# Optimization experiments

Measured on AMD Instinct MI355X. Metric: run time of the kernel, lower is better.

The kernel has to match this reference:

```python
import jax, jax.numpy as jnp
import numpy as np

N_HEADS = 16
EMBED = 1024
T = 2048        # given tokens
CACHE_NUM = 1024  # prepended cache tokens (x[0,-1] in the original)


def setup_inputs() -> dict:
    key = jax.random.key(0)
    k1, k2 = jax.random.split(key)
    qkv = jax.random.normal(k1, (T, 3 * EMBED), dtype=jnp.float32)
    # In the original these cache rows are torch.randn generated inside forward;
    # we lift them into a deterministic explicit input with identical semantics.
    cache = jax.random.normal(k2, (CACHE_NUM, 3 * EMBED), dtype=jnp.float32)
    return {"qkv": qkv, "cache": cache}


def reference(qkv, cache):
    C = EMBED
    H = N_HEADS
    D = C // H  # head_dim = 64
    t = qkv.shape[0]
    tc = cache.shape[0]
    t_full = t + tc  # T_ in the original

    gq, gk, gv = jnp.split(qkv, 3, axis=1)      # each [T, C]
    cq, ck, cv = jnp.split(cache, 3, axis=1)    # each [cache_num, C]

    q = jnp.concatenate([cq, gq], axis=0)  # [T_, C]
    k = jnp.concatenate([ck, gk], axis=0)
    v = jnp.concatenate([cv, gv], axis=0)

    # [T_, C] -> [H, T_, D]
    q = q.reshape(t_full, H, D).transpose(1, 0, 2)
    k = k.reshape(t_full, H, D).transpose(1, 0, 2)
    v = v.reshape(t_full, H, D).transpose(1, 0, 2)

    scale = 1.0 / np.sqrt(D).astype(np.float32)
    att = jnp.einsum('htd,hsd->hts', q, k) * scale  # [H, T_, T_]

    causal = jnp.tril(jnp.ones((t_full, t_full), dtype=bool))
    att = jnp.where(causal[None, :, :], att, jnp.float32(-jnp.inf))
    att = jax.nn.softmax(att, axis=-1)
    # attn_dropout is identity in eval / p=0

    y = jnp.einsum('hts,hsd->htd', att, v)          # [H, T_, D]
    y = y.transpose(1, 0, 2).reshape(t_full, C)     # [T_, C]
    return y[tc:, :]                                # drop cache rows -> [T, C]
```

## Files before the change

### kernel.cpp

```cpp
#include <hip/hip_runtime.h>
#include <cmath>


typedef _Float16 f16;
typedef __attribute__((ext_vector_type(8))) _Float16 f16x8;
typedef __attribute__((ext_vector_type(4))) _Float16 f16x4;
typedef __attribute__((ext_vector_type(2))) _Float16 f16x2;
typedef __attribute__((ext_vector_type(4))) float    f32x4;

constexpr int TC  = 1024;
constexpr int C3  = 3072;
constexpr int CE  = 1024;
constexpr int NH  = 16;
constexpr int TQ  = 2048;
constexpr int NKT = 48;

constexpr size_t KV_ELEMS = (size_t)NH * NKT * 4096;

constexpr int SPLITS[16] = {2,2,3,3,3,3,4,4,4,4,5,5,5,5,6,6};
constexpr int PRE[16]    = {0,2,4,7,10,13,16,20,24,28,32,37,42,47,52,58};
constexpr int NSLOT      = 64;

constexpr size_t OPART_E = (size_t)NSLOT * NH * 128 * 64;
constexpr size_t LPART_F = (size_t)NSLOT * NH * 128;

__device__ __forceinline__ void dma16(const void* g, void* l) {
    __builtin_amdgcn_global_load_lds(
        (const __attribute__((address_space(1))) void*)g,
        (__attribute__((address_space(3))) void*)l, 16, 0, 0);
}

__device__ __forceinline__ f16x2 pkrtz(float a, float b) {
    return __builtin_bit_cast(f16x2, __builtin_amdgcn_cvt_pkrtz(a, b));
}

__global__ __launch_bounds__(256)
void prepass_f16(const float* __restrict__ qkv, const float* __restrict__ cache,
                 f16* __restrict__ Kt, f16* __restrict__ Vt)
{
    const int b   = blockIdx.x;
    const int h   = b & 15;
    const int kt  = b >> 4;
    const int tid = threadIdx.x;
    const int bt  = kt * 64;
    const float* src = (bt < TC) ? (cache + (size_t)bt * C3)
                                 : (qkv + (size_t)(bt - TC) * C3);
    f16* ktile = Kt + (size_t)(h * NKT + kt) * 4096;
    f16* vtile = Vt + (size_t)(h * NKT + kt) * 4096;

    __shared__ f16 vtmp[64 * 66];

    {
        const int tok = tid >> 2;
        const int c4  = tid & 3;
        const float* p = src + (size_t)tok * C3 + h * 64 + CE + c4 * 16;
        f32x4 x0 = ((const f32x4*)p)[0], x1 = ((const f32x4*)p)[1];
        f32x4 x2 = ((const f32x4*)p)[2], x3 = ((const f32x4*)p)[3];
        const int ch0 = (2 * c4)     ^ (tok & 7);
        const int ch1 = (2 * c4 + 1) ^ (tok & 7);
        *(f16x8*)&ktile[tok * 64 + ch0 * 8] =
            (f16x8){(f16)x0.x,(f16)x0.y,(f16)x0.z,(f16)x0.w,
                    (f16)x1.x,(f16)x1.y,(f16)x1.z,(f16)x1.w};
        *(f16x8*)&ktile[tok * 64 + ch1 * 8] =
            (f16x8){(f16)x2.x,(f16)x2.y,(f16)x2.z,(f16)x2.w,
                    (f16)x3.x,(f16)x3.y,(f16)x3.z,(f16)x3.w};
    }
    {
        const int tok  = tid >> 2;
        const int dblk = (tid & 3) * 16;
        const float* p = src + (size_t)tok * C3 + h * 64 + 2 * CE + dblk;
        f32x4 x0 = ((const f32x4*)p)[0], x1 = ((const f32x4*)p)[1];
        f32x4 x2 = ((const f32x4*)p)[2], x3 = ((const f32x4*)p)[3];
        float v[16] = {x0.x,x0.y,x0.z,x0.w, x1.x,x1.y,x1.z,x1.w,
                       x2.x,x2.y,x2.z,x2.w, x3.x,x3.y,x3.z,x3.w};
        f16* dst = &vtmp[tok * 66 + dblk];
        #pragma unroll
        for (int i = 0; i < 8; ++i)
            *(f16x2*)&dst[2 * i] = (f16x2){(f16)v[2 * i], (f16)v[2 * i + 1]};
    }
    __syncthreads();
    {
        const int d  = tid >> 2;
        const int tb = (tid & 3) * 16;
        f16 col[16];
        #pragma unroll
        for (int i = 0; i < 16; ++i) col[i] = vtmp[(tb + i) * 66 + d];
        const int c0 = tb >> 3;
        *(f16x8*)&vtile[d * 64 + ((c0 ^ (d & 7)) * 8)] =
            (f16x8){col[0],col[1],col[2],col[3],col[4],col[5],col[6],col[7]};
        *(f16x8*)&vtile[d * 64 + (((c0 + 1) ^ (d & 7)) * 8)] =
            (f16x8){col[8],col[9],col[10],col[11],col[12],col[13],col[14],col[15]};
    }
}

__device__ __forceinline__ void tile_loop(
    const char* kg, const char* vg, int t0, int t1, int qbase_w,
    int l15, int quad, int ksw, int soff,
    const f16x8 (&qfrag)[2][2], f16 (&sKV)[2][8192],
    f32x4 (&o_accT)[2][4], float (&l_i)[2])
{
    {
        char* kl = (char*)&sKV[0][0]    + soff;
        char* vl = (char*)&sKV[0][4096] + soff;
        dma16(kg, kl);           dma16(kg + 1024, kl + 1024);
        dma16(vg, vl);           dma16(vg + 1024, vl + 1024);
    }
    int cur = 0;

    for (int kt = t0; kt < t1; ++kt) {
        asm volatile("s_waitcnt vmcnt(0) lgkmcnt(0)" ::: "memory");
        __syncthreads();

        kg += 8192; vg += 8192;
        if (kt + 1 < t1) {
            char* kl = (char*)&sKV[cur ^ 1][0]    + soff;
            char* vl = (char*)&sKV[cur ^ 1][4096] + soff;
            dma16(kg, kl);       dma16(kg + 1024, kl + 1024);
            dma16(vg, vl);       dma16(vg + 1024, vl + 1024);
        }
        const f16* sK  = &sKV[cur][0];
        const f16* sVT = &sKV[cur][4096];
        cur ^= 1;

        f32x4 sacc[2][4];
        #pragma unroll
        for (int u = 0; u < 2; ++u)
            #pragma unroll
            for (int kb = 0; kb < 4; ++kb) sacc[u][kb] = (f32x4){0.f,0.f,0.f,0.f};
        #pragma unroll
        for (int kb = 0; kb < 4; ++kb) {
            const int ib = (kb * 16 + l15) * 64 + ksw;
            f16x8 a0 = *(const f16x8*)&sK[ib];
            f16x8 a1 = *(const f16x8*)&sK[ib ^ 32];
            #pragma unroll
            for (int u = 0; u < 2; ++u) {
                sacc[u][kb] = __builtin_amdgcn_mfma_f32_16x16x32_f16(a0, qfrag[u][0], sacc[u][kb], 0, 0, 0);
                sacc[u][kb] = __builtin_amdgcn_mfma_f32_16x16x32_f16(a1, qfrag[u][1], sacc[u][kb], 0, 0, 0);
            }
        }

        if (kt * 64 + 63 > qbase_w) {
            #pragma unroll
            for (int u = 0; u < 2; ++u) {
                const int qg = qbase_w + u * 16 + l15;
                #pragma unroll
                for (int kb = 0; kb < 4; ++kb) {
                    const int kq = kt * 64 + kb * 16 + quad * 4;
                    #pragma unroll
                    for (int r = 0; r < 4; ++r)
                        if (kq + r > qg) sacc[u][kb][r] = -INFINITY;
                }
            }
        }

        f16x4 pfrag[2][4];
        #pragma unroll
        for (int u = 0; u < 2; ++u) {
            float ls = 0.f;
            #pragma unroll
            for (int kb = 0; kb < 4; ++kb) {
                const float p0 = exp2f(sacc[u][kb][0]);
                const float p1 = exp2f(sacc[u][kb][1]);
                const float p2 = exp2f(sacc[u][kb][2]);
                const float p3 = exp2f(sacc[u][kb][3]);
                ls += (p0 + p1) + (p2 + p3);
                f16x2 lo = pkrtz(p0, p1);
                f16x2 hi = pkrtz(p2, p3);
                pfrag[u][kb] = __builtin_shufflevector(lo, hi, 0, 1, 2, 3);
            }
            l_i[u] += ls;
        }

        #pragma unroll
        for (int dblk = 0; dblk < 4; ++dblk) {
            const int row = dblk * 16 + l15;
            #pragma unroll
            for (int kb = 0; kb < 4; ++kb) {
                const int ch = (kb * 2 + (quad >> 1)) ^ (row & 7);
                f16x4 vf = *(const f16x4*)
                    &sVT[row * 64 + ch * 8 + (quad & 1) * 4];
                #pragma unroll
                for (int u = 0; u < 2; ++u)
                    o_accT[u][dblk] = __builtin_amdgcn_mfma_f32_16x16x16f16(
                        vf, pfrag[u][kb], o_accT[u][dblk], 0, 0, 0);
            }
        }
    }
}

__global__ __launch_bounds__(256, 4)
void attn_splitk(const float* __restrict__ qkv,
                 const f16* __restrict__ Kt,
                 const f16* __restrict__ Vt,
                 f16*  __restrict__ Opart,
                 float* __restrict__ lpart)
{
    const int bb = blockIdx.x;
    const int h  = bb >> 6;
    const int g  = ((bb & 63) + h * 4) & 63;
    int qt = 0;
    #pragma unroll
    for (int i = 1; i < 16; ++i) qt += (g >= PRE[i]) ? 1 : 0;
    const int s   = g - PRE[qt];
    const int nsp = SPLITS[qt];
    const int nkt = 2 * qt + 18;
    const int t0  = nkt * s / nsp;
    const int t1  = nkt * (s + 1) / nsp;

    const int tid  = threadIdx.x;
    const int w    = tid >> 6;
    const int lane = tid & 63;
    const int l15  = lane & 15;
    const int quad = lane >> 4;

    __shared__ __align__(16) f16 sKV[2][8192];

    const float qs = 0.125f * 1.44269504088896f;
    f16x8 qfrag[2][2];
    #pragma unroll
    for (int u = 0; u < 2; ++u) {
        const float* qp = qkv + (size_t)(qt * 128 + w * 32 + u * 16 + l15) * C3
                              + h * 64 + quad * 8;
        #pragma unroll
        for (int c = 0; c < 2; ++c) {
            f32x4 a = *(const f32x4*)(qp + c * 32);
            f32x4 b = *(const f32x4*)(qp + c * 32 + 4);
            qfrag[u][c] = (f16x8){(f16)(a.x * qs), (f16)(a.y * qs),
                                  (f16)(a.z * qs), (f16)(a.w * qs),
                                  (f16)(b.x * qs), (f16)(b.y * qs),
                                  (f16)(b.z * qs), (f16)(b.w * qs)};
        }
    }

    f32x4 o_accT[2][4];
    #pragma unroll
    for (int u = 0; u < 2; ++u)
        #pragma unroll
        for (int d = 0; d < 4; ++d) o_accT[u][d] = (f32x4){0.f, 0.f, 0.f, 0.f};
    float l_i[2] = {0.f, 0.f};

    const int qbase_w = TC + qt * 128 + w * 32;
    const int soff = w * 2048 + lane * 16;
    const char* kg = (const char*)(Kt + (size_t)(h * NKT + t0) * 4096) + soff;
    const char* vg = (const char*)(Vt + (size_t)(h * NKT + t0) * 4096) + soff;
    const int ksw = (quad ^ (l15 & 7)) * 8;

    tile_loop(kg, vg, t0, t1, qbase_w, l15, quad, ksw, soff,
              qfrag, sKV, o_accT, l_i);

    #pragma unroll
    for (int u = 0; u < 2; ++u) {
        float lf = l_i[u];
        lf += __shfl_xor(lf, 16);
        lf += __shfl_xor(lf, 32);
        const int qloc = w * 32 + u * 16 + l15;
        const int slot = PRE[qt] + s;
        f16*   op = Opart + ((size_t)slot * NH + h) * (128 * 64);
        float* lp = lpart + ((size_t)slot * NH + h) * 128;
        #pragma unroll
        for (int dblk = 0; dblk < 4; ++dblk) {
            f32x4 o = o_accT[u][dblk];
            f16x2 lo = pkrtz(o.x, o.y);
            f16x2 hi = pkrtz(o.z, o.w);
            *(f16x4*)&op[qloc * 64 + dblk * 16 + quad * 4] =
                __builtin_shufflevector(lo, hi, 0, 1, 2, 3);
        }
        if (quad == 0) lp[qloc] = lf;
    }
}

__global__ __launch_bounds__(256)
void attn_direct(const float* __restrict__ qkv,
                 const f16* __restrict__ Kt,
                 const f16* __restrict__ Vt,
                 float* __restrict__ out)
{
    const int bb  = blockIdx.x;
    const int h   = bb & 15;
    const int idx = bb >> 4;
    const int qt  = (h < 8) ? idx : 15 - idx;
    const int nsp = SPLITS[qt];
    const int nkt = 2 * qt + 18;

    const int tid  = threadIdx.x;
    const int w    = tid >> 6;
    const int lane = tid & 63;
    const int l15  = lane & 15;
    const int quad = lane >> 4;

    __shared__ __align__(16) f16 sKV[2][8192];

    const float qs = 0.125f * 1.44269504088896f;
    f16x8 qfrag[2][2];
    #pragma unroll
    for (int u = 0; u < 2; ++u) {
        const float* qp = qkv + (size_t)(qt * 128 + w * 32 + u * 16 + l15) * C3
                              + h * 64 + quad * 8;
        #pragma unroll
        for (int c = 0; c < 2; ++c) {
            f32x4 a = *(const f32x4*)(qp + c * 32);
            f32x4 b = *(const f32x4*)(qp + c * 32 + 4);
            qfrag[u][c] = (f16x8){(f16)(a.x * qs), (f16)(a.y * qs),
                                  (f16)(a.z * qs), (f16)(a.w * qs),
                                  (f16)(b.x * qs), (f16)(b.y * qs),
                                  (f16)(b.z * qs), (f16)(b.w * qs)};
        }
    }

    const int qbase_w = TC + qt * 128 + w * 32;
    const int soff = w * 2048 + lane * 16;
    const char* kg0 = (const char*)(Kt + (size_t)h * NKT * 4096) + soff;
    const char* vg0 = (const char*)(Vt + (size_t)h * NKT * 4096) + soff;
    const int ksw = (quad ^ (l15 & 7)) * 8;

    f32x4 osum[2][4];
    #pragma unroll
    for (int u = 0; u < 2; ++u)
        #pragma unroll
        for (int d = 0; d < 4; ++d) osum[u][d] = (f32x4){0.f, 0.f, 0.f, 0.f};
    float lsum[2] = {0.f, 0.f};

    for (int s = 0; s < nsp; ++s) {
        if (s) __syncthreads();
        const int t0 = nkt * s / nsp;
        const int t1 = nkt * (s + 1) / nsp;

        f32x4 o_accT[2][4];
        #pragma unroll
        for (int u = 0; u < 2; ++u)
            #pragma unroll
            for (int d = 0; d < 4; ++d) o_accT[u][d] = (f32x4){0.f,0.f,0.f,0.f};
        float l_i[2] = {0.f, 0.f};

        tile_loop(kg0 + (size_t)t0 * 8192, vg0 + (size_t)t0 * 8192,
                  t0, t1, qbase_w, l15, quad, ksw, soff,
                  qfrag, sKV, o_accT, l_i);

        #pragma unroll
        for (int u = 0; u < 2; ++u) {
            float lf = l_i[u];
            lf += __shfl_xor(lf, 16);
            lf += __shfl_xor(lf, 32);
            lsum[u] += lf;
            #pragma unroll
            for (int dblk = 0; dblk < 4; ++dblk) {
                f32x4 o = o_accT[u][dblk];
                f16x2 lo = pkrtz(o.x, o.y);
                f16x2 hi = pkrtz(o.z, o.w);
                osum[u][dblk].x += (float)lo[0];
                osum[u][dblk].y += (float)lo[1];
                osum[u][dblk].z += (float)hi[0];
                osum[u][dblk].w += (float)hi[1];
            }
        }
    }

    #pragma unroll
    for (int u = 0; u < 2; ++u) {
        const float inv = 1.0f / lsum[u];
        const int qloc = w * 32 + u * 16 + l15;
        const int gq = qt * 128 + qloc;
        #pragma unroll
        for (int dblk = 0; dblk < 4; ++dblk) {
            f32x4 o = osum[u][dblk];
            *(f32x4*)&out[(size_t)gq * CE + h * 64 + dblk * 16 + quad * 4] =
                (f32x4){o.x * inv, o.y * inv, o.z * inv, o.w * inv};
        }
    }
}

__global__ __launch_bounds__(256)
void combine_splits(const f16* __restrict__ Opart,
                    const float* __restrict__ lpart,
                    float* __restrict__ out)
{
    const int t  = blockIdx.x * 256 + threadIdx.x;
    const int d4 = t & 15;
    const int q  = (t >> 4) & (TQ - 1);
    const int h  = t >> 15;

    const int qt    = q >> 7;
    const int qloc  = q & 127;
    const int nsp   = SPLITS[qt];
    const int slot0 = PRE[qt];

    float lsum = 0.f;
    f32x4 acc = (f32x4){0.f, 0.f, 0.f, 0.f};
    for (int s = 0; s < nsp; ++s) {
        const size_t sb = (size_t)(slot0 + s) * NH + h;
        lsum += lpart[sb * 128 + qloc];
        f16x4 o = *(const f16x4*)&Opart[sb * (128 * 64) + qloc * 64 + d4 * 4];
        acc.x += (float)o[0]; acc.y += (float)o[1];
        acc.z += (float)o[2]; acc.w += (float)o[3];
    }
    const float inv = 1.0f / lsum;
    *(f32x4*)&out[(size_t)q * CE + h * 64 + d4 * 4] =
        (f32x4){acc.x * inv, acc.y * inv, acc.z * inv, acc.w * inv};
}

extern "C" void kernel_launch(void* const* d_in, const int* in_sizes, int n_in,
                              void* d_out, int out_size, void* d_ws, size_t ws_size,
                              hipStream_t stream)
{
    const float* qkv   = (const float*)d_in[0];
    const float* cache = (const float*)d_in[1];
    float*       out   = (float*)d_out;
    (void)in_sizes; (void)n_in; (void)out_size;

    const size_t kv_bytes = 2 * KV_ELEMS * sizeof(f16);
    const size_t need     = kv_bytes + OPART_E * sizeof(f16)
                          + LPART_F * sizeof(float);

    f16*   Kt    = (f16*)d_ws;
    f16*   Vt    = Kt + KV_ELEMS;
    f16*   Opart = (f16*)((char*)d_ws + kv_bytes);
    float* lpart = (float*)((char*)Opart + OPART_E * sizeof(f16));

    const int split = (ws_size >= need) ? 1 : 0;

    prepass_f16<<<dim3(NH * NKT), dim3(256), 0, stream>>>(qkv, cache, Kt, Vt);
    if (split) {
        attn_splitk<<<dim3(1024), dim3(256), 0, stream>>>(qkv, Kt, Vt, Opart, lpart);
        combine_splits<<<dim3(NH * TQ * 16 / 256), dim3(256), 0, stream>>>(
            Opart, lpart, out);
    } else {
        attn_direct<<<dim3(256), dim3(256), 0, stream>>>(qkv, Kt, Vt, out);
    }
}
```

Measured before the change: 122.0 us.

## Software-pipeline QK-softmax with previous tile's PV and remap blocks per XCD

Restructures the attention tile loop so the QK^T plus softmax of tile k runs while the PV product of tile k-1 is issued. V tiles move into a triple buffer so the previous tile's V stays valid while the next one streams in, and the PV MFMA block runs at raised wave priority via s_setprio. Block indices in the prepass and split-K kernels are remapped so each XCD handles a fixed pair of heads, which is meant to improve L2 locality of the K/V tiles. The cost is extra LDS (5 tiles instead of 4) and extra registers to carry the previous P fragments, which could lower occupancy under the 4-blocks-per-CU launch bound.

```diff
diff --git a/kernel.cpp b/kernel.cpp
--- a/kernel.cpp
+++ b/kernel.cpp
@@ -39,8 +39,11 @@
                  f16* __restrict__ Kt, f16* __restrict__ Vt)
 {
     const int b   = blockIdx.x;
-    const int h   = b & 15;
-    const int kt  = b >> 4;
+    const int xcd = b & 7;
+    const int j   = b >> 3;
+    const int h   = xcd * 2 + ((j >= 48) ? 1 : 0);
+    const int kt  = (j >= 48) ? (j - 48) : j;
+
     const int tid = threadIdx.x;
     const int bt  = kt * 64;
     const float* src = (bt < TC) ? (cache + (size_t)bt * C3)
@@ -93,99 +96,130 @@
     }
 }
 
+__device__ __forceinline__ void qkt_softmax(
+    const f16* sKc, int kt, int qbase_w, int l15, int quad, int ksw,
+    const f16x8 (&qfrag)[2][2], f16x4 (&pf)[2][4], float (&l_i)[2])
+{
+    float ls0 = 0.f, ls1 = 0.f;
+    const bool diag = (kt * 64 + 63 > qbase_w);
+    #pragma unroll
+    for (int kb = 0; kb < 4; ++kb) {
+        const int ib = (kb * 16 + l15) * 64 + ksw;
+        f16x8 a0 = *(const f16x8*)&sKc[ib];
+        f16x8 a1 = *(const f16x8*)&sKc[ib ^ 32];
+        f32x4 sacc[2];
+        #pragma unroll
+        for (int u = 0; u < 2; ++u) {
+            f32x4 s = (f32x4){0.f, 0.f, 0.f, 0.f};
+            s = __builtin_amdgcn_mfma_f32_16x16x32_f16(a0, qfrag[u][0], s, 0, 0, 0);
+            s = __builtin_amdgcn_mfma_f32_16x16x32_f16(a1, qfrag[u][1], s, 0, 0, 0);
+            sacc[u] = s;
+        }
+        if (diag) {
+            #pragma unroll
+            for (int u = 0; u < 2; ++u) {
+                const int qg = qbase_w + u * 16 + l15;
+                const int kq = kt * 64 + kb * 16 + quad * 4;
+                #pragma unroll
+                for (int r = 0; r < 4; ++r)
+                    if (kq + r > qg) sacc[u][r] = -INFINITY;
+            }
+        }
+        #pragma unroll
+        for (int u = 0; u < 2; ++u) {
+            const float p0 = exp2f(sacc[u][0]);
+            const float p1 = exp2f(sacc[u][1]);
+            const float p2 = exp2f(sacc[u][2]);
+            const float p3 = exp2f(sacc[u][3]);
+            if (u == 0) ls0 += (p0 + p1) + (p2 + p3);
+            else        ls1 += (p0 + p1) + (p2 + p3);
+            f16x2 lo = pkrtz(p0, p1);
+            f16x2 hi = pkrtz(p2, p3);
+            pf[u][kb] = __builtin_shufflevector(lo, hi, 0, 1, 2, 3);
+        }
+    }
+    l_i[0] += ls0;
+    l_i[1] += ls1;
+}
+
+__device__ __forceinline__ void pv_accum(
+    const f16* sVT, int l15, int quad,
+    const f16x4 (&pf)[2][4], f32x4 (&o_accT)[2][4])
+{
+    __builtin_amdgcn_s_setprio(1);
+    #pragma unroll
+    for (int dblk = 0; dblk < 4; ++dblk) {
+        const int row = dblk * 16 + l15;
+        #pragma unroll
+        for (int kb = 0; kb < 4; ++kb) {
+            const int ch = (kb * 2 + (quad >> 1)) ^ (row & 7);
+            f16x4 vf = *(const f16x4*)&sVT[row * 64 + ch * 8 + (quad & 1) * 4];
+            #pragma unroll
+            for (int u = 0; u < 2; ++u)
+                o_accT[u][dblk] = __builtin_amdgcn_mfma_f32_16x16x16f16(
+                    vf, pf[u][kb], o_accT[u][dblk], 0, 0, 0);
+        }
+    }
+    __builtin_amdgcn_s_setprio(0);
+}
+
 __device__ __forceinline__ void tile_loop(
     const char* kg, const char* vg, int t0, int t1, int qbase_w,
     int l15, int quad, int ksw, int soff,
-    const f16x8 (&qfrag)[2][2], f16 (&sKV)[2][8192],
+    const f16x8 (&qfrag)[2][2],
+    f16 (&sK)[2][4096], f16 (&sV)[3][4096],
     f32x4 (&o_accT)[2][4], float (&l_i)[2])
 {
     {
-        char* kl = (char*)&sKV[0][0]    + soff;
-        char* vl = (char*)&sKV[0][4096] + soff;
-        dma16(kg, kl);           dma16(kg + 1024, kl + 1024);
-        dma16(vg, vl);           dma16(vg + 1024, vl + 1024);
-    }
-    int cur = 0;
-
-    for (int kt = t0; kt < t1; ++kt) {
+        char* kl = (char*)&sK[0][0] + soff;
+        char* vl = (char*)&sV[0][0] + soff;
+        dma16(kg, kl); dma16(kg + 1024, kl + 1024);
+        dma16(vg, vl); dma16(vg + 1024, vl + 1024);
+    }
+    f16x4 pfragP[2][4];
+    int kbuf, vbuf, vbufP;
+
+    {
         asm volatile("s_waitcnt vmcnt(0) lgkmcnt(0)" ::: "memory");
         __syncthreads();
-
         kg += 8192; vg += 8192;
+        if (t0 + 1 < t1) {
+            char* kl = (char*)&sK[1][0] + soff;
+            char* vl = (char*)&sV[1][0] + soff;
+            dma16(kg, kl); dma16(kg + 1024, kl + 1024);
+            dma16(vg, vl); dma16(vg + 1024, vl + 1024);
+        }
+        qkt_softmax(&sK[0][0], t0, qbase_w, l15, quad, ksw, qfrag, pfragP, l_i);
+        vbufP = 0; kbuf = 1; vbuf = 1;
+    }
+
+    for (int kt = t0 + 1; kt < t1; ++kt) {
+        asm volatile("s_waitcnt vmcnt(0) lgkmcnt(0)" ::: "memory");
+        __syncthreads();
+
+        kg += 8192; vg += 8192;
+        const int kbufN = kbuf ^ 1;
+        const int vbufN = (vbuf == 2) ? 0 : vbuf + 1;
         if (kt + 1 < t1) {
-            char* kl = (char*)&sKV[cur ^ 1][0]    + soff;
-            char* vl = (char*)&sKV[cur ^ 1][4096] + soff;
-            dma16(kg, kl);       dma16(kg + 1024, kl + 1024);
-            dma16(vg, vl);       dma16(vg + 1024, vl + 1024);
-        }
-        const f16* sK  = &sKV[cur][0];
-        const f16* sVT = &sKV[cur][4096];
-        cur ^= 1;
-
-        f32x4 sacc[2][4];
+            char* kl = (char*)&sK[kbufN][0] + soff;
+            char* vl = (char*)&sV[vbufN][0] + soff;
+            dma16(kg, kl); dma16(kg + 1024, kl + 1024);
+            dma16(vg, vl); dma16(vg + 1024, vl + 1024);
+        }
+
+        f16x4 pfragN[2][4];
+        qkt_softmax(&sK[kbuf][0], kt, qbase_w, l15, quad, ksw,
+                    qfrag, pfragN, l_i);
+        pv_accum(&sV[vbufP][0], l15, quad, pfragP, o_accT);
+
         #pragma unroll
         for (int u = 0; u < 2; ++u)
             #pragma unroll
-            for (int kb = 0; kb < 4; ++kb) sacc[u][kb] = (f32x4){0.f,0.f,0.f,0.f};
-        #pragma unroll
-        for (int kb = 0; kb < 4; ++kb) {
-            const int ib = (kb * 16 + l15) * 64 + ksw;
-            f16x8 a0 = *(const f16x8*)&sK[ib];
-            f16x8 a1 = *(const f16x8*)&sK[ib ^ 32];
-            #pragma unroll
-            for (int u = 0; u < 2; ++u) {
-                sacc[u][kb] = __builtin_amdgcn_mfma_f32_16x16x32_f16(a0, qfrag[u][0], sacc[u][kb], 0, 0, 0);
-                sacc[u][kb] = __builtin_amdgcn_mfma_f32_16x16x32_f16(a1, qfrag[u][1], sacc[u][kb], 0, 0, 0);
-            }
-        }
-
-        if (kt * 64 + 63 > qbase_w) {
-            #pragma unroll
-            for (int u = 0; u < 2; ++u) {
-                const int qg = qbase_w + u * 16 + l15;
-                #pragma unroll
-                for (int kb = 0; kb < 4; ++kb) {
-                    const int kq = kt * 64 + kb * 16 + quad * 4;
-                    #pragma unroll
-                    for (int r = 0; r < 4; ++r)
-                        if (kq + r > qg) sacc[u][kb][r] = -INFINITY;
-                }
-            }
-        }
-
-        f16x4 pfrag[2][4];
-        #pragma unroll
-        for (int u = 0; u < 2; ++u) {
-            float ls = 0.f;
-            #pragma unroll
-            for (int kb = 0; kb < 4; ++kb) {
-                const float p0 = exp2f(sacc[u][kb][0]);
-                const float p1 = exp2f(sacc[u][kb][1]);
-                const float p2 = exp2f(sacc[u][kb][2]);
-                const float p3 = exp2f(sacc[u][kb][3]);
-                ls += (p0 + p1) + (p2 + p3);
-                f16x2 lo = pkrtz(p0, p1);
-                f16x2 hi = pkrtz(p2, p3);
-                pfrag[u][kb] = __builtin_shufflevector(lo, hi, 0, 1, 2, 3);
-            }
-            l_i[u] += ls;
-        }
-
-        #pragma unroll
-        for (int dblk = 0; dblk < 4; ++dblk) {
-            const int row = dblk * 16 + l15;
-            #pragma unroll
-            for (int kb = 0; kb < 4; ++kb) {
-                const int ch = (kb * 2 + (quad >> 1)) ^ (row & 7);
-                f16x4 vf = *(const f16x4*)
-                    &sVT[row * 64 + ch * 8 + (quad & 1) * 4];
-                #pragma unroll
-                for (int u = 0; u < 2; ++u)
-                    o_accT[u][dblk] = __builtin_amdgcn_mfma_f32_16x16x16f16(
-                        vf, pfrag[u][kb], o_accT[u][dblk], 0, 0, 0);
-            }
-        }
-    }
+            for (int kb = 0; kb < 4; ++kb) pfragP[u][kb] = pfragN[u][kb];
+        vbufP = vbuf; kbuf = kbufN; vbuf = vbufN;
+    }
+
+    pv_accum(&sV[vbufP][0], l15, quad, pfragP, o_accT);
 }
 
 __global__ __launch_bounds__(256, 4)
@@ -196,8 +230,10 @@
                  float* __restrict__ lpart)
 {
     const int bb = blockIdx.x;
-    const int h  = bb >> 6;
-    const int g  = ((bb & 63) + h * 4) & 63;
+    const int xcd = bb & 7;
+    const int j   = bb >> 3;
+    const int h   = xcd * 2 + (j >> 6);
+    const int g   = j & 63;
     int qt = 0;
     #pragma unroll
     for (int i = 1; i < 16; ++i) qt += (g >= PRE[i]) ? 1 : 0;
@@ -213,7 +249,8 @@
     const int l15  = lane & 15;
     const int quad = lane >> 4;
 
-    __shared__ __align__(16) f16 sKV[2][8192];
+    __shared__ __align__(16) f16 sK[2][4096];
+    __shared__ __align__(16) f16 sV[3][4096];
 
     const float qs = 0.125f * 1.44269504088896f;
     f16x8 qfrag[2][2];
@@ -246,7 +283,7 @@
     const int ksw = (quad ^ (l15 & 7)) * 8;
 
     tile_loop(kg, vg, t0, t1, qbase_w, l15, quad, ksw, soff,
-              qfrag, sKV, o_accT, l_i);
+              qfrag, sK, sV, o_accT, l_i);
 
     #pragma unroll
     for (int u = 0; u < 2; ++u) {
@@ -288,7 +325,8 @@
     const int l15  = lane & 15;
     const int quad = lane >> 4;
 
-    __shared__ __align__(16) f16 sKV[2][8192];
+    __shared__ __align__(16) f16 sK[2][4096];
+    __shared__ __align__(16) f16 sV[3][4096];
 
     const float qs = 0.125f * 1.44269504088896f;
     f16x8 qfrag[2][2];
@@ -334,7 +372,7 @@
 
         tile_loop(kg0 + (size_t)t0 * 8192, vg0 + (size_t)t0 * 8192,
                   t0, t1, qbase_w, l15, quad, ksw, soff,
-                  qfrag, sKV, o_accT, l_i);
+                  qfrag, sK, sV, o_accT, l_i);
 
         #pragma unroll
         for (int u = 0; u < 2; ++u) {
```

New measurement: 135.4 us. 11.0% more time.
